# Kernel optimization log

Measured on AMD Instinct MI355X. Metric: run time of the kernel, lower is better.

The kernel has to match this reference:

```python
import jax, jax.numpy as jnp
import numpy as np

N_HEADS = 8


def _norm_weights(idx):
    # softmax over where(idx>0, 1, -9e15) along axis 1 -> uniform weights over non-pad slots
    logits = jnp.where(idx > 0, jnp.float32(1.0), jnp.float32(-9e15))
    return jax.nn.softmax(logits, axis=1)


def _layer_norm(x, g, b, eps=1e-6):
    mu = jnp.mean(x, axis=-1, keepdims=True)
    var = jnp.var(x, axis=-1, keepdims=True)
    return (x - mu) * jax.lax.rsqrt(var + eps) * g + b


def _mha_block(x, mask, wq, wk, wv, wo, g, b):
    # standard multi-head self-attention block with residual + layernorm
    B, L, D = x.shape
    hd = D // N_HEADS
    q = (x @ wq).reshape(B, L, N_HEADS, hd)
    k = (x @ wk).reshape(B, L, N_HEADS, hd)
    v = (x @ wv).reshape(B, L, N_HEADS, hd)
    scores = jnp.einsum('bqhd,bkhd->bhqk', q, k) / jnp.float32(np.sqrt(hd))
    scores = jnp.where(mask[:, None, None, :], jnp.float32(-1e9), scores)
    attn = jax.nn.softmax(scores, axis=-1)
    out = jnp.einsum('bhqk,bkhd->bqhd', attn, v).reshape(B, L, D) @ wo
    return _layer_norm(out + x, g, b)


def _forward(data_idx, seq, timestamps, user_level, useq, user_inf, user_cen,
             spread_status, id2vector,
             user_emb, cen_emb, time_emb, pos_emb, inf_emb,
             w1, w2, w3,
             t_wq, t_wk, t_wv, t_wo, t_g, t_b,
             s_wq, s_wk, s_wv, s_wo, s_g, s_b,
             W, W2, f_l1_w, f_l1_b, f_l2_w, f_l2_b, lin_w, lin_b):
    # ---- HGNN layer (hypergraph conv) ----
    tv = w3[0]  # TextVector = weight3[0]
    dot = w3 @ tv
    cos = dot / (jnp.linalg.norm(tv) * jnp.linalg.norm(w3, axis=1))
    inter_nw = jnp.mean(cos)  # scalar

    tweet_hidden = user_emb + cen_emb[user_cen]          # [N, D]
    x = (tweet_hidden @ w1) * inter_nw                   # [N, D]
    nor = _norm_weights(seq)                             # [E, L]
    edge = jnp.einsum('elc,el->ec', x[seq], nor)         # gather + weighted reduce
    edge = jax.nn.relu(edge)
    e1 = edge @ w2                                       # [E, D]
    u_nor = _norm_weights(useq)                          # [N, Lu]
    node = jnp.einsum('nlc,nl->nc', e1[useq], u_nor)     # [N, D]

    # ---- HGSL head ----
    sb = seq[data_idx]                                   # [B, L]
    nor_b = _norm_weights(sb)
    att_mask = sb == 0                                   # PAD == 0
    adj = node[sb]                                       # [B, L, D]

    att_hidden = adj + time_emb[timestamps[data_idx]]
    att_out = _mha_block(att_hidden, att_mask, t_wq, t_wk, t_wv, t_wo, t_g, t_b)
    news = jnp.einsum('blc,bl->bc', att_out, nor_b)
    news = jnp.concatenate([news, spread_status[data_idx][:, 2:] / 3600.0 / 24.0], axis=-1) @ W

    att_hidden_s = adj + inf_emb[user_inf[data_idx]] + pos_emb[user_level[data_idx]]
    att_out_s = _mha_block(att_hidden_s, att_mask, s_wq, s_wk, s_wv, s_wo, s_g, s_b)
    news_s = jnp.einsum('blc,bl->bc', att_out_s, nor_b)
    news_s = jnp.concatenate([news_s, spread_status[data_idx][:, :2]], axis=-1) @ W2

    # Gated fusion (linear3 unused in original forward; id2vector is overwritten/unused)
    emb = jnp.stack([news, news_s], axis=0)              # [2, B, D+2]
    score = jax.nn.softmax(jnp.tanh(emb @ f_l1_w + f_l1_b) @ f_l2_w + f_l2_b, axis=0)
    fused = jnp.sum(score * emb, axis=0)                 # [B, D+2]
    return jax.nn.log_softmax(fused @ lin_w + lin_b, axis=1)


def setup_inputs():
    key = jax.random.key(0)
    ks = jax.random.split(key, 40)
    N, E, L, Lu, D, B, TV = 50000, 10000, 50, 20, 128, 512, 768
    Dw = D + 2
    s = 0.05
    inp = {
        'data_idx': jax.random.randint(ks[0], (B,), 0, E),
        'seq': jax.random.randint(ks[1], (E, L), 0, N),
        'timestamps': jax.random.randint(ks[2], (E, L), 0, 5000),
        'user_level': jax.random.randint(ks[3], (E, L), 0, 50),
        'useq': jax.random.randint(ks[4], (N, Lu), 0, E),
        'user_inf': jax.random.randint(ks[5], (E, L), 0, 200),
        'user_cen': jax.random.randint(ks[6], (N,), 0, 600),
        'spread_status': jax.random.uniform(ks[7], (E, 4), dtype=jnp.float32),
        'id2vector': jax.random.normal(ks[8], (1,), dtype=jnp.float32),
        'user_emb': s * jax.random.normal(ks[9], (N, D), dtype=jnp.float32),
        'cen_emb': s * jax.random.normal(ks[10], (600, D), dtype=jnp.float32),
        'time_emb': s * jax.random.normal(ks[11], (5000, D), dtype=jnp.float32),
        'pos_emb': s * jax.random.normal(ks[12], (50, D), dtype=jnp.float32),
        'inf_emb': s * jax.random.normal(ks[13], (200, D), dtype=jnp.float32),
        'w1': s * jax.random.normal(ks[14], (D, D), dtype=jnp.float32),
        'w2': s * jax.random.normal(ks[15], (D, D), dtype=jnp.float32),
        'w3': s * jax.random.normal(ks[16], (TV, TV), dtype=jnp.float32),
        'W': s * jax.random.normal(ks[17], (Dw, Dw), dtype=jnp.float32),
        'W2': s * jax.random.normal(ks[18], (Dw, Dw), dtype=jnp.float32),
        'f_l1_w': s * jax.random.normal(ks[19], (Dw, Dw), dtype=jnp.float32),
        'f_l1_b': jnp.zeros((Dw,), jnp.float32),
        'f_l2_w': s * jax.random.normal(ks[20], (Dw, 1), dtype=jnp.float32),
        'f_l2_b': jnp.zeros((1,), jnp.float32),
        'lin_w': s * jax.random.normal(ks[21], (Dw, 2), dtype=jnp.float32),
        'lin_b': jnp.zeros((2,), jnp.float32),
    }
    for nm, i in [('t', 22), ('s', 27)]:
        inp[nm + '_wq'] = s * jax.random.normal(ks[i], (D, D), dtype=jnp.float32)
        inp[nm + '_wk'] = s * jax.random.normal(ks[i + 1], (D, D), dtype=jnp.float32)
        inp[nm + '_wv'] = s * jax.random.normal(ks[i + 2], (D, D), dtype=jnp.float32)
        inp[nm + '_wo'] = s * jax.random.normal(ks[i + 3], (D, D), dtype=jnp.float32)
        inp[nm + '_g'] = jnp.ones((D,), jnp.float32)
        inp[nm + '_b'] = jnp.zeros((D,), jnp.float32)
    return inp


def reference(data_idx, seq, timestamps, user_level, useq, user_inf, user_cen,
              spread_status, id2vector,
              user_emb, cen_emb, time_emb, pos_emb, inf_emb,
              w1, w2, w3,
              t_wq, t_wk, t_wv, t_wo, t_g, t_b,
              s_wq, s_wk, s_wv, s_wo, s_g, s_b,
              W, W2, f_l1_w, f_l1_b, f_l2_w, f_l2_b, lin_w, lin_b):
    return _forward(data_idx, seq, timestamps, user_level, useq, user_inf, user_cen,
                    spread_status, id2vector,
                    user_emb, cen_emb, time_emb, pos_emb, inf_emb,
                    w1, w2, w3,
                    t_wq, t_wk, t_wv, t_wo, t_g, t_b,
                    s_wq, s_wk, s_wv, s_wo, s_g, s_b,
                    W, W2, f_l1_w, f_l1_b, f_l2_w, f_l2_b, lin_w, lin_b)
```

## Files before the change

### kernel.cpp

```cpp
#include <hip/hip_runtime.h>
#include <math.h>

constexpr int Nn = 50000;
constexpr int Ee = 10000;
constexpr int Ll = 50;
constexpr int LuU = 20;
constexpr int Dd = 128;
constexpr int Bb = 512;
constexpr int TVv = 768;
constexpr int Dw = 130;
constexpr int BL = Bb * Ll;
constexpr int BLP = Bb * 64;

typedef __attribute__((ext_vector_type(8))) short bf8v;
typedef __attribute__((ext_vector_type(4))) float f4v;
typedef __attribute__((ext_vector_type(8))) unsigned short u16x8;
typedef __attribute__((ext_vector_type(4))) unsigned short u16x4;

__device__ __forceinline__ unsigned short f2bf(float f) {
  union { float f; unsigned u; } v; v.f = f;
  unsigned r = v.u + 0x7FFFu + ((v.u >> 16) & 1u);
  return (unsigned short)(r >> 16);
}
__device__ __forceinline__ float bf2f(unsigned short h) {
  union { unsigned u; float f; } v; v.u = ((unsigned)h) << 16; return v.f;
}
__device__ __forceinline__ int swz(int b) { return b ^ (((b >> 8) & 7) << 4); }
__device__ __forceinline__ int swz7(int b) { return b ^ (((b >> 7) & 7) << 4); }

__device__ __forceinline__ float block_sum_256(float v, volatile float* scr) {
#pragma unroll
  for (int o = 32; o > 0; o >>= 1) v += __shfl_down(v, o, 64);
  __syncthreads();
  if ((threadIdx.x & 63) == 0) scr[threadIdx.x >> 6] = v;
  __syncthreads();
  return scr[0] + scr[1] + scr[2] + scr[3];
}

__global__ __launch_bounds__(256) void k_cos(const float* __restrict__ w3,
                                             float* __restrict__ dotb,
                                             float* __restrict__ nrmb) {
  __shared__ float scr[4];
  int i = blockIdx.x;
  const float* row = w3 + (size_t)i * TVv;
  float d = 0.f, n = 0.f;
  for (int j = threadIdx.x; j < TVv; j += 256) {
    float a = row[j];
    d += a * w3[j];
    n += a * a;
  }
  d = block_sum_256(d, scr);
  n = block_sum_256(n, scr);
  if (threadIdx.x == 0) { dotb[i] = d; nrmb[i] = n; }
}

__global__ __launch_bounds__(256) void k_internw(const float* __restrict__ dotb,
                                                 const float* __restrict__ nrmb,
                                                 float* __restrict__ internw) {
  __shared__ float scr[4];
  float n0 = sqrtf(nrmb[0]);
  float s = 0.f;
  for (int i = threadIdx.x; i < TVv; i += 256)
    s += dotb[i] / (n0 * sqrtf(nrmb[i]));
  s = block_sum_256(s, scr);
  if (threadIdx.x == 0) *internw = s / (float)TVv;
}

__global__ __launch_bounds__(256) void k_prep(
    const float* w1, const float* w2,
    const float* twq, const float* twk, const float* twv, const float* two,
    const float* swq, const float* swk, const float* swv, const float* swo,
    unsigned short* __restrict__ out) {
  int wsel = blockIdx.x >> 3, part = blockIdx.x & 7;
  const float* w;
  switch (wsel) {
    case 0: w = w1; break;  case 1: w = w2; break;
    case 2: w = twq; break; case 3: w = twk; break;
    case 4: w = twv; break; case 5: w = two; break;
    case 6: w = swq; break; case 7: w = swk; break;
    case 8: w = swv; break; default: w = swo; break;
  }
  int u = part * 256 + threadIdx.x;
  int n = u >> 4, k0 = (u & 15) * 8;
  u16x8 pv;
#pragma unroll
  for (int i = 0; i < 8; i++) pv[i] = f2bf(w[(size_t)(k0 + i) * Dd + n]);
  ((u16x8*)(out + (size_t)wsel * Dd * Dd))[u] = pv;
}

template <int MODE>
__global__ __launch_bounds__(256) void k_gemm_plain(
    const void* __restrict__ inA, const float* __restrict__ in1,
    const int* __restrict__ gidx, const float* __restrict__ scalep,
    const unsigned short* __restrict__ WTg,
    unsigned short* __restrict__ out, int nrows) {
  __shared__ unsigned short WT[Dd * Dd];
  __shared__ __align__(16) unsigned short Ab[64 * Dd];
  int tid = threadIdx.x;
  {
    const u16x8* src = (const u16x8*)WTg;
    for (int u = tid; u < 2048; u += 256)
      *(u16x8*)((char*)WT + swz(u * 16)) = src[u];
  }
  int r0 = blockIdx.x * 64;
  if constexpr (MODE == 0) {
    float sc = *scalep;
    for (int u = tid; u < 1024; u += 256) {
      int rr = u >> 4, c0 = (u & 15) * 8;
      int r = r0 + rr;
      u16x8 pv;
      if (r < nrows) {
        const float* a = (const float*)inA + (size_t)r * Dd + c0;
        const float* c = in1 + (size_t)gidx[r] * Dd + c0;
#pragma unroll
        for (int i = 0; i < 8; i++) pv[i] = f2bf((a[i] + c[i]) * sc);
      } else {
#pragma unroll
        for (int i = 0; i < 8; i++) pv[i] = 0;
      }
      *(u16x8*)((char*)Ab + swz(rr * 256 + c0 * 2)) = pv;
    }
  } else {
    for (int u = tid; u < 1024; u += 256) {
      int rr = u >> 4;
      int r = r0 + rr;
      u16x8 pv;
      if (r < nrows) pv = ((const u16x8*)inA)[(size_t)r * 16 + (u & 15)];
      else {
#pragma unroll
        for (int i = 0; i < 8; i++) pv[i] = 0;
      }
      *(u16x8*)((char*)Ab + swz(rr * 256 + (u & 15) * 16)) = pv;
    }
  }
  __syncthreads();
  int lane = tid & 63, wid = tid >> 6;
  int lrow = lane & 15, lg = lane >> 4;
  bf8v af[4];
#pragma unroll
  for (int kc = 0; kc < 4; kc++)
    af[kc] = *(const bf8v*)((char*)Ab + swz((wid * 16 + lrow) * 256 + kc * 64 + lg * 16));
  f4v acc[8];
#pragma unroll
  for (int nt = 0; nt < 8; nt++)
#pragma unroll
    for (int j = 0; j < 4; j++) acc[nt][j] = 0.f;
#pragma unroll
  for (int nt = 0; nt < 8; nt++)
#pragma unroll
    for (int kc = 0; kc < 4; kc++) {
      bf8v bfg = *(const bf8v*)((char*)WT + swz((nt * 16 + lrow) * 256 + kc * 64 + lg * 16));
      acc[nt] = __builtin_amdgcn_mfma_f32_16x16x32_bf16(af[kc], bfg, acc[nt], 0, 0, 0);
    }
#pragma unroll
  for (int nt = 0; nt < 8; nt++)
#pragma unroll
    for (int j = 0; j < 4; j++) {
      int r = r0 + wid * 16 + lg * 4 + j;
      if (r < nrows) out[(size_t)r * Dd + nt * 16 + lrow] = f2bf(acc[nt][j]);
    }
}

__global__ __launch_bounds__(256) void k_gemm_qkv(
    const unsigned short* __restrict__ hidT, const unsigned short* __restrict__ hidS,
    const unsigned short* __restrict__ WTbase,
    unsigned short* __restrict__ Qp, unsigned short* __restrict__ Kp,
    unsigned short* __restrict__ VTp) {
  __shared__ unsigned short WT[Dd * Dd];
  __shared__ __align__(16) unsigned short Ab[128 * Dd];
  int tile = blockIdx.x & 255, branch = blockIdx.x >> 8;
  const unsigned short* in = branch ? hidS : hidT;
  int tid = threadIdx.x;
  for (int u = tid; u < 2048; u += 256) {
    int rr = u >> 4, ch = u & 15;
    int brow = rr >> 6, sub = rr & 63;
    u16x8 pv;
    if (sub < Ll)
      pv = ((const u16x8*)in)[(size_t)((tile * 2 + brow) * Ll + sub) * 16 + ch];
    else {
#pragma unroll
      for (int i = 0; i < 8; i++) pv[i] = 0;
    }
    *(u16x8*)((char*)Ab + swz(rr * 256 + ch * 16)) = pv;
  }
  {
    const u16x8* srcW = (const u16x8*)(WTbase + (size_t)(2 + branch * 4) * Dd * Dd);
    for (int u = tid; u < 2048; u += 256)
      *(u16x8*)((char*)WT + swz(u * 16)) = srcW[u];
  }
  __syncthreads();
  int lane = tid & 63, wid = tid >> 6;
  int lrow = lane & 15, lg = lane >> 4;
  bf8v af[2][4];
#pragma unroll
  for (int mi = 0; mi < 2; mi++)
#pragma unroll
    for (int kc = 0; kc < 4; kc++)
      af[mi][kc] = *(const bf8v*)((char*)Ab +
                    swz((wid * 32 + mi * 16 + lrow) * 256 + kc * 64 + lg * 16));
#pragma unroll 1
  for (int sel = 0; sel < 3; sel++) {
    f4v acc[2][8];
#pragma unroll
    for (int mi = 0; mi < 2; mi++)
#pragma unroll
      for (int nt = 0; nt < 8; nt++)
#pragma unroll
        for (int j = 0; j < 4; j++) acc[mi][nt][j] = 0.f;
#pragma unroll
    for (int nt = 0; nt < 8; nt++)
#pragma unroll
      for (int kc = 0; kc < 4; kc++) {
        bf8v bfg = *(const bf8v*)((char*)WT + swz((nt * 16 + lrow) * 256 + kc * 64 + lg * 16));
        acc[0][nt] = __builtin_amdgcn_mfma_f32_16x16x32_bf16(af[0][kc], bfg, acc[0][nt], 0, 0, 0);
        acc[1][nt] = __builtin_amdgcn_mfma_f32_16x16x32_bf16(af[1][kc], bfg, acc[1][nt], 0, 0, 0);
      }
    if (sel < 2) {
      unsigned short* outb = ((sel == 0) ? Qp : Kp) + (size_t)branch * BLP * Dd;
#pragma unroll
      for (int mi = 0; mi < 2; mi++)
#pragma unroll
        for (int nt = 0; nt < 8; nt++)
#pragma unroll
          for (int j = 0; j < 4; j++) {
            int r = tile * 128 + wid * 32 + mi * 16 + lg * 4 + j;
            outb[(size_t)r * Dd + nt * 16 + lrow] = f2bf(acc[mi][nt][j]);
          }
      __syncthreads();
      const u16x8* srcW = (const u16x8*)(WTbase + (size_t)(2 + branch * 4 + sel + 1) * Dd * Dd);
      for (int u = tid; u < 2048; u += 256)
        *(u16x8*)((char*)WT + swz(u * 16)) = srcW[u];
      __syncthreads();
    } else {
      __syncthreads();
#pragma unroll
      for (int mi = 0; mi < 2; mi++)
#pragma unroll
        for (int nt = 0; nt < 8; nt++) {
          int d = nt * 16 + lrow;
          int rl = wid * 32 + mi * 16 + lg * 4;
          u16x4 tv;
#pragma unroll
          for (int j = 0; j < 4; j++) tv[j] = f2bf(acc[mi][nt][j]);
          *(u16x4*)((char*)Ab + swz(d * 256 + rl * 2)) = tv;
        }
      __syncthreads();
      for (int u = tid; u < 2048; u += 256) {
        int d = u >> 4, ch = u & 15;
        u16x8 pv = *(const u16x8*)((char*)Ab + swz(d * 256 + ch * 16));
        int bidx = ch >> 3, kv0 = (ch & 7) * 8;
        *(u16x8*)(VTp + (((size_t)branch * Bb + tile * 2 + bidx) * Dd + d) * 64 + kv0) = pv;
      }
    }
  }
}

__global__ __launch_bounds__(256) void k_gemm_ln(
    const unsigned short* __restrict__ ctxp,
    const unsigned short* __restrict__ hidT, const unsigned short* __restrict__ hidS,
    const unsigned short* __restrict__ WTbase,
    const float* __restrict__ tg, const float* __restrict__ tb,
    const float* __restrict__ sg, const float* __restrict__ sb_,
    unsigned short* __restrict__ attall) {
  __shared__ unsigned short WT[Dd * Dd];
  __shared__ __align__(16) char UB[64 * 132 * 4];
  unsigned short* Ab = (unsigned short*)UB;
  float (*O)[132] = (float (*)[132])UB;

  int b = blockIdx.x & 511, branch = blockIdx.x >> 9;
  const unsigned short* resid = (branch ? hidS : hidT);
  const unsigned short* Wg = WTbase + (size_t)(5 + branch * 4) * Dd * Dd;
  const float* lng = branch ? sg : tg;
  const float* lnb = branch ? sb_ : tb;
  unsigned short* out = attall + (size_t)branch * BL * Dd;
  int tid = threadIdx.x;

  {
    const u16x8* src = (const u16x8*)Wg;
    for (int u = tid; u < 2048; u += 256)
      *(u16x8*)((char*)WT + swz(u * 16)) = src[u];
  }
  for (int u = tid; u < 1024; u += 256) {
    int rr = u >> 4;
    u16x8 pv = ((const u16x8*)ctxp)[(((size_t)branch * Bb + b) * 64 + rr) * 16 + (u & 15)];
    *(u16x8*)((char*)Ab + swz(rr * 256 + (u & 15) * 16)) = pv;
  }
  __syncthreads();

  int lane = tid & 63, wid = tid >> 6;
  int lrow = lane & 15, lg = lane >> 4;
  bf8v af[4];
#pragma unroll
  for (int kc = 0; kc < 4; kc++)
    af[kc] = *(const bf8v*)((char*)Ab + swz((wid * 16 + lrow) * 256 + kc * 64 + lg * 16));
  f4v acc[8];
#pragma unroll
  for (int nt = 0; nt < 8; nt++)
#pragma unroll
    for (int j = 0; j < 4; j++) acc[nt][j] = 0.f;
#pragma unroll
  for (int nt = 0; nt < 8; nt++)
#pragma unroll
    for (int kc = 0; kc < 4; kc++) {
      bf8v bfg = *(const bf8v*)((char*)WT + swz((nt * 16 + lrow) * 256 + kc * 64 + lg * 16));
      acc[nt] = __builtin_amdgcn_mfma_f32_16x16x32_bf16(af[kc], bfg, acc[nt], 0, 0, 0);
    }
  __syncthreads();
#pragma unroll
  for (int nt = 0; nt < 8; nt++)
#pragma unroll
    for (int j = 0; j < 4; j++)
      O[wid * 16 + lg * 4 + j][nt * 16 + lrow] = acc[nt][j];
  __syncthreads();
  int r = tid >> 2, c0 = (tid & 3) * 32;
  if (r < Ll) {
    size_t gr = (size_t)b * Ll + r;
    float vv[32];
    float s1 = 0.f, s2 = 0.f;
#pragma unroll
    for (int i8 = 0; i8 < 4; i8++) {
      u16x8 hb = *(const u16x8*)(resid + gr * Dd + c0 + i8 * 8);
#pragma unroll
      for (int i = 0; i < 8; i++) {
        float x = O[r][c0 + i8 * 8 + i] + bf2f(hb[i]);
        vv[i8 * 8 + i] = x; s1 += x; s2 += x * x;
      }
    }
    s1 += __shfl_xor(s1, 1, 64); s2 += __shfl_xor(s2, 1, 64);
    s1 += __shfl_xor(s1, 2, 64); s2 += __shfl_xor(s2, 2, 64);
    float mu = s1 * (1.f / Dd);
    float var = s2 * (1.f / Dd) - mu * mu;
    float rs = rsqrtf(var + 1e-6f);
#pragma unroll
    for (int i8 = 0; i8 < 4; i8++) {
      u16x8 ov;
#pragma unroll
      for (int i = 0; i < 8; i++) {
        int c = c0 + i8 * 8 + i;
        ov[i] = f2bf((vv[i8 * 8 + i] - mu) * rs * lng[c] + lnb[c]);
      }
      *(u16x8*)(out + gr * Dd + c0 + i8 * 8) = ov;
    }
  }
}

__global__ __launch_bounds__(256) void k_gather_e(const unsigned short* __restrict__ X,
                                                  const int* __restrict__ seq,
                                                  unsigned short* __restrict__ EDGE) {
  int r = blockIdx.x * 16 + (threadIdx.x >> 4);
  int c0 = (threadIdx.x & 15) * 8;
  const int* row = seq + (size_t)r * Ll;
  float acc[8];
#pragma unroll
  for (int i = 0; i < 8; i++) acc[i] = 0.f;
  int cnt = 0;
#pragma unroll 1
  for (int l0 = 0; l0 < Ll; l0 += 10) {
    int ids[10];
#pragma unroll
    for (int t = 0; t < 10; t++) ids[t] = row[l0 + t];
    u16x8 vv[10];
#pragma unroll
    for (int t = 0; t < 10; t++)
      vv[t] = *(const u16x8*)(X + (size_t)ids[t] * Dd + c0);
#pragma unroll
    for (int t = 0; t < 10; t++)
      if (ids[t] > 0) {
        cnt++;
#pragma unroll
        for (int i = 0; i < 8; i++) acc[i] += bf2f(vv[t][i]);
      }
  }
  u16x8 ov;
  if (cnt) {
    float inv = 1.f / (float)cnt;
#pragma unroll
    for (int i = 0; i < 8; i++) ov[i] = f2bf(fmaxf(acc[i] * inv, 0.f));
  } else {
    u16x8 x0 = *(const u16x8*)(X + c0);
#pragma unroll
    for (int i = 0; i < 8; i++) ov[i] = f2bf(fmaxf(bf2f(x0[i]), 0.f));
  }
  *(u16x8*)(EDGE + (size_t)r * Dd + c0) = ov;
}

__global__ __launch_bounds__(256) void k_hidfuse(
    const unsigned short* __restrict__ E1, const int* __restrict__ data_idx,
    const int* __restrict__ seq, const int* __restrict__ tsmp,
    const int* __restrict__ uinf, const int* __restrict__ ulev,
    const int* __restrict__ useq,
    const float* __restrict__ time_emb, const float* __restrict__ inf_emb,
    const float* __restrict__ pos_emb,
    unsigned short* __restrict__ hidTb, unsigned short* __restrict__ hidSb) {
  int bl = blockIdx.x * 16 + (threadIdx.x >> 4);
  int c0 = (threadIdx.x & 15) * 8;
  int b = bl / Ll, l = bl % Ll;
  int e = data_idx[b];
  int sid = seq[(size_t)e * Ll + l];
  const int* urow = useq + (size_t)sid * LuU;
  float acc[8];
#pragma unroll
  for (int i = 0; i < 8; i++) acc[i] = 0.f;
  int cnt = 0;
#pragma unroll 1
  for (int t0 = 0; t0 < LuU; t0 += 10) {
    int ids[10];
#pragma unroll
    for (int t = 0; t < 10; t++) ids[t] = urow[t0 + t];
    u16x8 vv[10];
#pragma unroll
    for (int t = 0; t < 10; t++)
      vv[t] = *(const u16x8*)(E1 + (size_t)ids[t] * Dd + c0);
#pragma unroll
    for (int t = 0; t < 10; t++)
      if (ids[t] > 0) {
        cnt++;
#pragma unroll
        for (int i = 0; i < 8; i++) acc[i] += bf2f(vv[t][i]);
      }
  }
  float node[8];
  if (cnt) {
    float inv = 1.f / (float)cnt;
#pragma unroll
    for (int i = 0; i < 8; i++) node[i] = acc[i] * inv;
  } else {
    u16x8 e0 = *(const u16x8*)(E1 + c0);
#pragma unroll
    for (int i = 0; i < 8; i++) node[i] = bf2f(e0[i]);
  }
  int ts = tsmp[(size_t)e * Ll + l];
  int fi = uinf[(size_t)e * Ll + l];
  int lv = ulev[(size_t)e * Ll + l];
  const float4* tp = (const float4*)(time_emb + (size_t)ts * Dd + c0);
  const float4* ip = (const float4*)(inf_emb + (size_t)fi * Dd + c0);
  const float4* pp = (const float4*)(pos_emb + (size_t)lv * Dd + c0);
  float4 t0 = tp[0], t1 = tp[1];
  float4 i0 = ip[0], i1 = ip[1];
  float4 p0 = pp[0], p1 = pp[1];
  float te[8] = {t0.x, t0.y, t0.z, t0.w, t1.x, t1.y, t1.z, t1.w};
  float ie[8] = {i0.x, i0.y, i0.z, i0.w, i1.x, i1.y, i1.z, i1.w};
  float pe[8] = {p0.x, p0.y, p0.z, p0.w, p1.x, p1.y, p1.z, p1.w};
  u16x8 ht, hs;
#pragma unroll
  for (int i = 0; i < 8; i++) {
    ht[i] = f2bf(node[i] + te[i]);
    hs[i] = f2bf(node[i] + ie[i] + pe[i]);
  }
  size_t o = (size_t)bl * Dd + c0;
  *(u16x8*)(hidTb + o) = ht;
  *(u16x8*)(hidSb + o) = hs;
}

__global__ __launch_bounds__(256, 4) void k_attn_mfma(
    const unsigned short* __restrict__ Qp,
    const unsigned short* __restrict__ Kp,
    const unsigned short* __restrict__ VTp,
    const int* __restrict__ data_idx,
    const int* __restrict__ seq,
    unsigned short* __restrict__ ctxp) {
  __shared__ __align__(16) char PTs[4 * 8192];
  __shared__ int maskl[Ll];
  int b = blockIdx.x, branch = blockIdx.y;
  int tid = threadIdx.x, lane = tid & 63, wid = tid >> 6;
  if (tid < Ll) maskl[tid] = (seq[(size_t)data_idx[b] * Ll + tid] == 0);
  __syncthreads();
  int lrow = lane & 15, lg = lane >> 4;
  size_t rbase = ((size_t)branch * Bb + b) * 64;
  size_t vrow  = ((size_t)branch * Bb + b) * Dd;
  char* PTw = PTs + wid * 8192;
#pragma unroll 1
  for (int hi = 0; hi < 2; hi++) {
    int h = wid * 2 + hi;
    bf8v af[4], bq[4];
    if (lg < 2) {
#pragma unroll
      for (int t = 0; t < 4; t++) {
        af[t] = *(const bf8v*)(Kp + (rbase + t * 16 + lrow) * Dd + h * 16 + lg * 8);
        bq[t] = *(const bf8v*)(Qp + (rbase + t * 16 + lrow) * Dd + h * 16 + lg * 8);
      }
    } else {
#pragma unroll
      for (int t = 0; t < 4; t++)
#pragma unroll
        for (int i = 0; i < 8; i++) { af[t][i] = 0; bq[t][i] = 0; }
    }
#pragma unroll 1
    for (int nt = 0; nt < 4; nt++) {
      f4v sa[4];
#pragma unroll
      for (int mt = 0; mt < 4; mt++)
#pragma unroll
        for (int j = 0; j < 4; j++) sa[mt][j] = 0.f;
#pragma unroll
      for (int mt = 0; mt < 4; mt++)
        sa[mt] = __builtin_amdgcn_mfma_f32_16x16x32_bf16(af[mt], bq[nt], sa[mt], 0, 0, 0);
      float m = -3.0e38f;
#pragma unroll
      for (int mt = 0; mt < 4; mt++)
#pragma unroll
        for (int j = 0; j < 4; j++) {
          int kk = mt * 16 + lg * 4 + j;
          int mk = (kk < Ll) ? maskl[kk] : 2;
          float v = sa[mt][j] * 0.25f;
          v = (mk == 1) ? -1e9f : v;
          v = (mk == 2) ? -3.0e38f : v;
          sa[mt][j] = v;
          m = fmaxf(m, v);
        }
      m = fmaxf(m, __shfl_xor(m, 16, 64));
      m = fmaxf(m, __shfl_xor(m, 32, 64));
      float s = 0.f;
#pragma unroll
      for (int mt = 0; mt < 4; mt++)
#pragma unroll
        for (int j = 0; j < 4; j++) {
          float p = expf(sa[mt][j] - m);
          sa[mt][j] = p;
          s += p;
        }
      s += __shfl_xor(s, 16, 64);
      s += __shfl_xor(s, 32, 64);
      float inv = 1.f / s;
      int q = nt * 16 + lrow;
#pragma unroll
      for (int mt = 0; mt < 4; mt++) {
        u16x4 pw;
#pragma unroll
        for (int j = 0; j < 4; j++) pw[j] = f2bf(sa[mt][j] * inv);
        *(u16x4*)(PTw + swz7(q * 128 + mt * 32 + lg * 8)) = pw;
      }
    }
    f4v pacc[4];
#pragma unroll
    for (int nt = 0; nt < 4; nt++)
#pragma unroll
      for (int j = 0; j < 4; j++) pacc[nt][j] = 0.f;
#pragma unroll
    for (int kt = 0; kt < 2; kt++) {
      bf8v av = *(const bf8v*)(VTp + (vrow + h * 16 + lrow) * 64 + kt * 32 + lg * 8);
#pragma unroll
      for (int nt = 0; nt < 4; nt++) {
        bf8v bv = *(const bf8v*)(PTw + swz7((nt * 16 + lrow) * 128 + kt * 64 + lg * 16));
        pacc[nt] = __builtin_amdgcn_mfma_f32_16x16x32_bf16(av, bv, pacc[nt], 0, 0, 0);
      }
    }
#pragma unroll
    for (int nt = 0; nt < 4; nt++) {
      int q = nt * 16 + lrow;
      unsigned* cp = (unsigned*)(ctxp + (rbase + q) * Dd + h * 16 + lg * 4);
      cp[0] = (unsigned)f2bf(pacc[nt][0]) | ((unsigned)f2bf(pacc[nt][1]) << 16);
      cp[1] = (unsigned)f2bf(pacc[nt][2]) | ((unsigned)f2bf(pacc[nt][3]) << 16);
    }
  }
}

__global__ __launch_bounds__(128) void k_newsred(const unsigned short* __restrict__ attall,
                                                 const int* __restrict__ data_idx,
                                                 const int* __restrict__ seq,
                                                 const float* __restrict__ spread,
                                                 float* __restrict__ news) {
  __shared__ int sl[Ll];
  __shared__ int scnt;
  int b = blockIdx.x, branch = blockIdx.y;
  int e = data_idx[b];
  const unsigned short* att = attall + (size_t)branch * BL * Dd;
  if (threadIdx.x < Ll) sl[threadIdx.x] = seq[(size_t)e * Ll + threadIdx.x];
  __syncthreads();
  if (threadIdx.x == 0) {
    int c = 0;
    for (int l = 0; l < Ll; l++) c += (sl[l] > 0);
    scnt = c;
  }
  __syncthreads();
  int cnt = scnt;
  float wnp = cnt ? 1.f / (float)cnt : 0.02f;
  int c = threadIdx.x;
  float acc = 0.f;
  for (int l = 0; l < Ll; l++) {
    float w = cnt ? ((sl[l] > 0) ? wnp : 0.f) : wnp;
    acc += w * bf2f(att[((size_t)b * Ll + l) * Dd + c]);
  }
  float* nrow = news + ((size_t)branch * Bb + b) * 132;
  nrow[c] = acc;
  if (c < 2) {
    nrow[Dd + c] = branch ? spread[(size_t)e * 4 + c]
                          : spread[(size_t)e * 4 + 2 + c] * (1.f / 86400.f);
  }
}

__global__ __launch_bounds__(256) void k_newsW(const float* __restrict__ news,
                                               const float* __restrict__ Wm,
                                               const float* __restrict__ W2m,
                                               float* __restrict__ NT,
                                               float* __restrict__ NS) {
  __shared__ float Wl[Dw][Dw + 1];
  __shared__ float nrow[132];
  int branch = blockIdx.y;
  const float* W = branch ? W2m : Wm;
  float* out = branch ? NS : NT;
  for (int u = threadIdx.x; u < Dw * Dw; u += 256)
    Wl[u / Dw][u % Dw] = W[u];
  for (int rr = 0; rr < 32; rr++) {
    int b = blockIdx.x * 32 + rr;
    __syncthreads();
    if (threadIdx.x < Dw)
      nrow[threadIdx.x] = news[((size_t)branch * Bb + b) * 132 + threadIdx.x];
    __syncthreads();
    int j = threadIdx.x;
    if (j < Dw) {
      float acc = 0.f;
      for (int kk = 0; kk < Dw; kk++) acc += nrow[kk] * Wl[kk][j];
      out[(size_t)b * Dw + j] = acc;
    }
  }
}

__global__ __launch_bounds__(256) void k_fusion(const float* __restrict__ nt,
                                                const float* __restrict__ ns,
                                                const float* __restrict__ l1w,
                                                const float* __restrict__ l1b,
                                                const float* __restrict__ l2w,
                                                const float* __restrict__ l2b,
                                                const float* __restrict__ linw,
                                                const float* __restrict__ linb,
                                                float* __restrict__ out) {
  __shared__ float rt[Dw], rs[Dw];
  __shared__ float scr[4];
  int b = blockIdx.x, j = threadIdx.x;
  if (j < Dw) { rt[j] = nt[(size_t)b * Dw + j]; rs[j] = ns[(size_t)b * Dw + j]; }
  __syncthreads();
  float pt = 0.f, ps = 0.f;
  if (j < Dw) {
    float at = l1b[j], as = l1b[j];
    for (int kk = 0; kk < Dw; kk++) {
      float w = l1w[(size_t)kk * Dw + j];
      at += rt[kk] * w;
      as += rs[kk] * w;
    }
    float lw2 = l2w[j];
    pt = tanhf(at) * lw2;
    ps = tanhf(as) * lw2;
  }
  float st = block_sum_256(pt, scr);
  float ss = block_sum_256(ps, scr);
  st += l2b[0]; ss += l2b[0];
  float m = fmaxf(st, ss);
  float e0 = expf(st - m), e1v = expf(ss - m);
  float inv = 1.f / (e0 + e1v);
  float s0 = e0 * inv, s1 = e1v * inv;
  float fj  = (j < Dw) ? (s0 * rt[j] + s1 * rs[j]) : 0.f;
  float w0  = (j < Dw) ? linw[(size_t)j * 2 + 0] : 0.f;
  float w1v = (j < Dw) ? linw[(size_t)j * 2 + 1] : 0.f;
  float l0 = block_sum_256(fj * w0, scr);
  float l1 = block_sum_256(fj * w1v, scr);
  if (j == 0) {
    l0 += linb[0]; l1 += linb[1];
    float mm = fmaxf(l0, l1);
    float lse = mm + logf(expf(l0 - mm) + expf(l1 - mm));
    out[(size_t)b * 2 + 0] = l0 - lse;
    out[(size_t)b * 2 + 1] = l1 - lse;
  }
}

extern "C" void kernel_launch(void* const* d_in, const int* in_sizes, int n_in,
                              void* d_out, int out_size, void* d_ws, size_t ws_size,
                              hipStream_t stream) {
  const int*   data_idx = (const int*)d_in[0];
  const int*   seq      = (const int*)d_in[1];
  const int*   tsmp     = (const int*)d_in[2];
  const int*   ulev     = (const int*)d_in[3];
  const int*   useq     = (const int*)d_in[4];
  const int*   uinf     = (const int*)d_in[5];
  const int*   ucen     = (const int*)d_in[6];
  const float* spread   = (const float*)d_in[7];
  const float* user_emb = (const float*)d_in[9];
  const float* cen_emb  = (const float*)d_in[10];
  const float* time_emb = (const float*)d_in[11];
  const float* pos_emb  = (const float*)d_in[12];
  const float* inf_emb  = (const float*)d_in[13];
  const float* w1       = (const float*)d_in[14];
  const float* w2       = (const float*)d_in[15];
  const float* w3       = (const float*)d_in[16];
  const float* Wm       = (const float*)d_in[17];
  const float* W2m      = (const float*)d_in[18];
  const float* f_l1_w   = (const float*)d_in[19];
  const float* f_l1_b   = (const float*)d_in[20];
  const float* f_l2_w   = (const float*)d_in[21];
  const float* f_l2_b   = (const float*)d_in[22];
  const float* lin_w    = (const float*)d_in[23];
  const float* lin_b    = (const float*)d_in[24];
  const float* t_wq = (const float*)d_in[25];
  const float* t_wk = (const float*)d_in[26];
  const float* t_wv = (const float*)d_in[27];
  const float* t_wo = (const float*)d_in[28];
  const float* t_g  = (const float*)d_in[29];
  const float* t_b  = (const float*)d_in[30];
  const float* s_wq = (const float*)d_in[31];
  const float* s_wk = (const float*)d_in[32];
  const float* s_wv = (const float*)d_in[33];
  const float* s_wo = (const float*)d_in[34];
  const float* s_g  = (const float*)d_in[35];
  const float* s_b  = (const float*)d_in[36];

  char* ws = (char*)d_ws;
  constexpr size_t SZ_WT  = (size_t)10 * Dd * Dd * 2;
  constexpr size_t SZ_XB  = (size_t)Nn * Dd * 2;
  constexpr size_t SZ_EB  = (size_t)Ee * Dd * 2;
  constexpr size_t SZ_BH  = (size_t)BL * Dd * 2;
  constexpr size_t SZ_PD  = (size_t)2 * BLP * Dd * 2;
  constexpr size_t OFF_WT  = 8192;
  constexpr size_t OFF_X   = OFF_WT + SZ_WT;
  constexpr size_t OFF_EDGE= OFF_X + SZ_XB;
  constexpr size_t OFF_E1  = OFF_EDGE + SZ_EB;
  constexpr size_t OFF_HTB = OFF_E1 + SZ_EB;
  constexpr size_t OFF_HSB = OFF_HTB + SZ_BH;
  constexpr size_t OFF_Q   = OFF_HSB + SZ_BH;
  constexpr size_t OFF_K   = OFF_Q + SZ_PD;
  constexpr size_t OFF_VT  = OFF_K + SZ_PD;
  constexpr size_t OFF_CTX = OFF_VT + SZ_PD;
  constexpr size_t OFF_ATT = OFF_Q;
  constexpr size_t OFF_NEWS= OFF_CTX + SZ_PD;
  constexpr size_t OFF_NT  = OFF_NEWS + (size_t)2 * Bb * 132 * 4;
  constexpr size_t OFF_NS  = OFF_NT + (size_t)Bb * Dw * 4;

  float* dotb    = (float*)(ws + 0);
  float* nrmb    = (float*)(ws + 3072);
  float* internw = (float*)(ws + 6144);
  unsigned short* WTall = (unsigned short*)(ws + OFF_WT);
  unsigned short* Xb    = (unsigned short*)(ws + OFF_X);
  unsigned short* EDGEb = (unsigned short*)(ws + OFF_EDGE);
  unsigned short* E1b   = (unsigned short*)(ws + OFF_E1);
  unsigned short* HIDTb = (unsigned short*)(ws + OFF_HTB);
  unsigned short* HIDSb = (unsigned short*)(ws + OFF_HSB);
  unsigned short* Qp    = (unsigned short*)(ws + OFF_Q);
  unsigned short* Kp    = (unsigned short*)(ws + OFF_K);
  unsigned short* VTp   = (unsigned short*)(ws + OFF_VT);
  unsigned short* CTXp  = (unsigned short*)(ws + OFF_CTX);
  unsigned short* ATTall= (unsigned short*)(ws + OFF_ATT);
  float*          NEWS  = (float*)(ws + OFF_NEWS);
  float*          NT    = (float*)(ws + OFF_NT);
  float*          NS    = (float*)(ws + OFF_NS);
  float* outp = (float*)d_out;

  k_prep<<<80, 256, 0, stream>>>(w1, w2, t_wq, t_wk, t_wv, t_wo,
                                 s_wq, s_wk, s_wv, s_wo, WTall);
  k_cos<<<TVv, 256, 0, stream>>>(w3, dotb, nrmb);
  k_internw<<<1, 256, 0, stream>>>(dotb, nrmb, internw);

  k_gemm_plain<0><<<(Nn + 63) / 64, 256, 0, stream>>>(
      user_emb, cen_emb, ucen, internw, WTall + 0 * Dd * Dd, Xb, Nn);
  k_gather_e<<<Ee / 16, 256, 0, stream>>>(Xb, seq, EDGEb);
  k_gemm_plain<1><<<(Ee + 63) / 64, 256, 0, stream>>>(
      EDGEb, nullptr, nullptr, nullptr, WTall + 1 * Dd * Dd, E1b, Ee);
  k_hidfuse<<<BL / 16, 256, 0, stream>>>(E1b, data_idx, seq, tsmp, uinf, ulev, useq,
                                         time_emb, inf_emb, pos_emb, HIDTb, HIDSb);

  k_gemm_qkv<<<512, 256, 0, stream>>>(HIDTb, HIDSb, WTall, Qp, Kp, VTp);
  k_attn_mfma<<<dim3(Bb, 2), 256, 0, stream>>>(Qp, Kp, VTp, data_idx, seq, CTXp);
  k_gemm_ln<<<1024, 256, 0, stream>>>(CTXp, HIDTb, HIDSb, WTall,
                                      t_g, t_b, s_g, s_b, ATTall);

  k_newsred<<<dim3(Bb, 2), 128, 0, stream>>>(ATTall, data_idx, seq, spread, NEWS);
  k_newsW<<<dim3(16, 2), 256, 0, stream>>>(NEWS, Wm, W2m, NT, NS);
  k_fusion<<<Bb, 256, 0, stream>>>(NT, NS, f_l1_w, f_l1_b, f_l2_w, f_l2_b,
                                   lin_w, lin_b, outp);

  (void)in_sizes; (void)n_in; (void)out_size; (void)ws_size;
}
```

Baseline: 378.1 us.

## Fuse QKV projection and attention into one per-sequence kernel

Merges the QKV GEMM kernel and the attention kernel into a single kernel with one block per (batch, branch). Q, K and V^T stay in LDS instead of round-tripping through global memory, and the mask is built through lane shuffles rather than an LDS table. In exchange, each block now reloads all three 128x128 weight matrices for only 64 rows, and the 80KB of LDS caps occupancy at about two blocks per CU.

```diff
diff --git a/kernel.cpp b/kernel.cpp
--- a/kernel.cpp
+++ b/kernel.cpp
@@ -161,96 +161,216 @@
     }
 }
 
-__global__ __launch_bounds__(256) void k_gemm_qkv(
+__global__ __launch_bounds__(256, 2) void k_qkvattn(
     const unsigned short* __restrict__ hidT, const unsigned short* __restrict__ hidS,
     const unsigned short* __restrict__ WTbase,
-    unsigned short* __restrict__ Qp, unsigned short* __restrict__ Kp,
-    unsigned short* __restrict__ VTp) {
-  __shared__ unsigned short WT[Dd * Dd];
-  __shared__ __align__(16) unsigned short Ab[128 * Dd];
-  int tile = blockIdx.x & 255, branch = blockIdx.x >> 8;
-  const unsigned short* in = branch ? hidS : hidT;
-  int tid = threadIdx.x;
-  for (int u = tid; u < 2048; u += 256) {
+    const int* __restrict__ data_idx, const int* __restrict__ seq,
+    unsigned short* __restrict__ ctxp) {
+  __shared__ __align__(16) char LDS[81920];
+  unsigned short* AQ  = (unsigned short*)(LDS);
+  unsigned short* WP  = (unsigned short*)(LDS + 16384);
+  unsigned short* Ks  = (unsigned short*)(LDS + 49152);
+  unsigned short* VTs = (unsigned short*)(LDS + 65536);
+
+  int b = blockIdx.x, branch = blockIdx.y;
+  int tid = threadIdx.x, lane = tid & 63, wid = tid >> 6;
+  int lrow = lane & 15, lg = lane >> 4;
+  const unsigned short* hid = (branch ? hidS : hidT) + (size_t)b * Ll * Dd;
+
+  int e = data_idx[b];
+  int mi = (lane < Ll) ? (seq[(size_t)e * Ll + lane] == 0 ? 1 : 0) : 2;
+  int mflag[4][4];
+#pragma unroll
+  for (int mt = 0; mt < 4; mt++)
+#pragma unroll
+    for (int j = 0; j < 4; j++)
+      mflag[mt][j] = __shfl(mi, mt * 16 + lg * 4 + j, 64);
+
+  for (int u = tid; u < 1024; u += 256) {
     int rr = u >> 4, ch = u & 15;
-    int brow = rr >> 6, sub = rr & 63;
     u16x8 pv;
-    if (sub < Ll)
-      pv = ((const u16x8*)in)[(size_t)((tile * 2 + brow) * Ll + sub) * 16 + ch];
+    if (rr < Ll) pv = *(const u16x8*)(hid + (size_t)rr * Dd + ch * 8);
     else {
 #pragma unroll
       for (int i = 0; i < 8; i++) pv[i] = 0;
     }
-    *(u16x8*)((char*)Ab + swz(rr * 256 + ch * 16)) = pv;
+    *(u16x8*)((char*)AQ + swz(rr * 256 + ch * 16)) = pv;
   }
   {
     const u16x8* srcW = (const u16x8*)(WTbase + (size_t)(2 + branch * 4) * Dd * Dd);
     for (int u = tid; u < 2048; u += 256)
-      *(u16x8*)((char*)WT + swz(u * 16)) = srcW[u];
-  }
-  __syncthreads();
-  int lane = tid & 63, wid = tid >> 6;
-  int lrow = lane & 15, lg = lane >> 4;
-  bf8v af[2][4];
-#pragma unroll
-  for (int mi = 0; mi < 2; mi++)
-#pragma unroll
-    for (int kc = 0; kc < 4; kc++)
-      af[mi][kc] = *(const bf8v*)((char*)Ab +
-                    swz((wid * 32 + mi * 16 + lrow) * 256 + kc * 64 + lg * 16));
+      *(u16x8*)((char*)WP + swz(u * 16)) = srcW[u];
+  }
+  __syncthreads();
+  bf8v hf[4];
+#pragma unroll
+  for (int kc = 0; kc < 4; kc++)
+    hf[kc] = *(const bf8v*)((char*)AQ + swz((wid * 16 + lrow) * 256 + kc * 64 + lg * 16));
+  __syncthreads();
+
+  {
+    f4v acc[8];
+#pragma unroll
+    for (int nt = 0; nt < 8; nt++)
+#pragma unroll
+      for (int j = 0; j < 4; j++) acc[nt][j] = 0.f;
+#pragma unroll
+    for (int nt = 0; nt < 8; nt++)
+#pragma unroll
+      for (int kc = 0; kc < 4; kc++) {
+        bf8v wf = *(const bf8v*)((char*)WP + swz((nt * 16 + lrow) * 256 + kc * 64 + lg * 16));
+        acc[nt] = __builtin_amdgcn_mfma_f32_16x16x32_bf16(wf, hf[kc], acc[nt], 0, 0, 0);
+      }
+    __syncthreads();
+#pragma unroll
+    for (int nt = 0; nt < 8; nt++) {
+      u16x4 qv;
+#pragma unroll
+      for (int j = 0; j < 4; j++) qv[j] = f2bf(acc[nt][j]);
+      *(u16x4*)((char*)AQ + swz((wid * 16 + lrow) * 256 + (nt * 16 + lg * 4) * 2)) = qv;
+    }
+  }
+  {
+    const u16x8* srcW = (const u16x8*)(WTbase + (size_t)(3 + branch * 4) * Dd * Dd);
+    for (int u = tid; u < 2048; u += 256)
+      *(u16x8*)((char*)WP + swz(u * 16)) = srcW[u];
+  }
+  __syncthreads();
+  {
+    f4v acc[8];
+#pragma unroll
+    for (int nt = 0; nt < 8; nt++)
+#pragma unroll
+      for (int j = 0; j < 4; j++) acc[nt][j] = 0.f;
+#pragma unroll
+    for (int nt = 0; nt < 8; nt++)
+#pragma unroll
+      for (int kc = 0; kc < 4; kc++) {
+        bf8v wf = *(const bf8v*)((char*)WP + swz((nt * 16 + lrow) * 256 + kc * 64 + lg * 16));
+        acc[nt] = __builtin_amdgcn_mfma_f32_16x16x32_bf16(wf, hf[kc], acc[nt], 0, 0, 0);
+      }
+    __syncthreads();
+#pragma unroll
+    for (int nt = 0; nt < 8; nt++) {
+      u16x4 kv4;
+#pragma unroll
+      for (int j = 0; j < 4; j++) kv4[j] = f2bf(acc[nt][j]);
+      *(u16x4*)((char*)Ks + swz((wid * 16 + lrow) * 256 + (nt * 16 + lg * 4) * 2)) = kv4;
+    }
+  }
+  {
+    const u16x8* srcW = (const u16x8*)(WTbase + (size_t)(4 + branch * 4) * Dd * Dd);
+    for (int u = tid; u < 2048; u += 256)
+      *(u16x8*)((char*)WP + swz(u * 16)) = srcW[u];
+  }
+  __syncthreads();
+  {
+    f4v acc[8];
+#pragma unroll
+    for (int nt = 0; nt < 8; nt++)
+#pragma unroll
+      for (int j = 0; j < 4; j++) acc[nt][j] = 0.f;
+#pragma unroll
+    for (int nt = 0; nt < 8; nt++)
+#pragma unroll
+      for (int kc = 0; kc < 4; kc++) {
+        bf8v wf = *(const bf8v*)((char*)WP + swz((nt * 16 + lrow) * 256 + kc * 64 + lg * 16));
+        acc[nt] = __builtin_amdgcn_mfma_f32_16x16x32_bf16(hf[kc], wf, acc[nt], 0, 0, 0);
+      }
+    __syncthreads();
+#pragma unroll
+    for (int nt = 0; nt < 8; nt++) {
+      u16x4 tv;
+#pragma unroll
+      for (int j = 0; j < 4; j++) tv[j] = f2bf(acc[nt][j]);
+      *(u16x4*)((char*)VTs + swz7((nt * 16 + lrow) * 128 + (wid * 16 + lg * 4) * 2)) = tv;
+    }
+  }
+  __syncthreads();
+
+  char* PTw = (char*)WP + wid * 8192;
+  size_t rbase = ((size_t)branch * Bb + b) * 64;
 #pragma unroll 1
-  for (int sel = 0; sel < 3; sel++) {
-    f4v acc[2][8];
-#pragma unroll
-    for (int mi = 0; mi < 2; mi++)
-#pragma unroll
-      for (int nt = 0; nt < 8; nt++)
-#pragma unroll
-        for (int j = 0; j < 4; j++) acc[mi][nt][j] = 0.f;
-#pragma unroll
-    for (int nt = 0; nt < 8; nt++)
-#pragma unroll
-      for (int kc = 0; kc < 4; kc++) {
-        bf8v bfg = *(const bf8v*)((char*)WT + swz((nt * 16 + lrow) * 256 + kc * 64 + lg * 16));
-        acc[0][nt] = __builtin_amdgcn_mfma_f32_16x16x32_bf16(af[0][kc], bfg, acc[0][nt], 0, 0, 0);
-        acc[1][nt] = __builtin_amdgcn_mfma_f32_16x16x32_bf16(af[1][kc], bfg, acc[1][nt], 0, 0, 0);
-      }
-    if (sel < 2) {
-      unsigned short* outb = ((sel == 0) ? Qp : Kp) + (size_t)branch * BLP * Dd;
-#pragma unroll
-      for (int mi = 0; mi < 2; mi++)
-#pragma unroll
-        for (int nt = 0; nt < 8; nt++)
-#pragma unroll
-          for (int j = 0; j < 4; j++) {
-            int r = tile * 128 + wid * 32 + mi * 16 + lg * 4 + j;
-            outb[(size_t)r * Dd + nt * 16 + lrow] = f2bf(acc[mi][nt][j]);
-          }
-      __syncthreads();
-      const u16x8* srcW = (const u16x8*)(WTbase + (size_t)(2 + branch * 4 + sel + 1) * Dd * Dd);
-      for (int u = tid; u < 2048; u += 256)
-        *(u16x8*)((char*)WT + swz(u * 16)) = srcW[u];
-      __syncthreads();
+  for (int hi = 0; hi < 2; hi++) {
+    int h = wid * 2 + hi;
+    bf8v af[4], bq[4];
+    if (lg < 2) {
+#pragma unroll
+      for (int t = 0; t < 4; t++) {
+        af[t] = *(const bf8v*)((char*)Ks + swz((t * 16 + lrow) * 256 + h * 32 + lg * 16));
+        bq[t] = *(const bf8v*)((char*)AQ + swz((t * 16 + lrow) * 256 + h * 32 + lg * 16));
+      }
     } else {
-      __syncthreads();
-#pragma unroll
-      for (int mi = 0; mi < 2; mi++)
-#pragma unroll
-        for (int nt = 0; nt < 8; nt++) {
-          int d = nt * 16 + lrow;
-          int rl = wid * 32 + mi * 16 + lg * 4;
-          u16x4 tv;
-#pragma unroll
-          for (int j = 0; j < 4; j++) tv[j] = f2bf(acc[mi][nt][j]);
-          *(u16x4*)((char*)Ab + swz(d * 256 + rl * 2)) = tv;
+#pragma unroll
+      for (int t = 0; t < 4; t++)
+#pragma unroll
+        for (int i = 0; i < 8; i++) { af[t][i] = 0; bq[t][i] = 0; }
+    }
+#pragma unroll 1
+    for (int nt = 0; nt < 4; nt++) {
+      f4v sa[4];
+#pragma unroll
+      for (int mt = 0; mt < 4; mt++)
+#pragma unroll
+        for (int j = 0; j < 4; j++) sa[mt][j] = 0.f;
+#pragma unroll
+      for (int mt = 0; mt < 4; mt++)
+        sa[mt] = __builtin_amdgcn_mfma_f32_16x16x32_bf16(af[mt], bq[nt], sa[mt], 0, 0, 0);
+      float m = -3.0e38f;
+#pragma unroll
+      for (int mt = 0; mt < 4; mt++)
+#pragma unroll
+        for (int j = 0; j < 4; j++) {
+          int mk = mflag[mt][j];
+          float v = sa[mt][j] * 0.25f;
+          v = (mk == 1) ? -1e9f : v;
+          v = (mk == 2) ? -3.0e38f : v;
+          sa[mt][j] = v;
+          m = fmaxf(m, v);
         }
-      __syncthreads();
-      for (int u = tid; u < 2048; u += 256) {
-        int d = u >> 4, ch = u & 15;
-        u16x8 pv = *(const u16x8*)((char*)Ab + swz(d * 256 + ch * 16));
-        int bidx = ch >> 3, kv0 = (ch & 7) * 8;
-        *(u16x8*)(VTp + (((size_t)branch * Bb + tile * 2 + bidx) * Dd + d) * 64 + kv0) = pv;
-      }
+      m = fmaxf(m, __shfl_xor(m, 16, 64));
+      m = fmaxf(m, __shfl_xor(m, 32, 64));
+      float s = 0.f;
+#pragma unroll
+      for (int mt = 0; mt < 4; mt++)
+#pragma unroll
+        for (int j = 0; j < 4; j++) {
+          float p = expf(sa[mt][j] - m);
+          sa[mt][j] = p;
+          s += p;
+        }
+      s += __shfl_xor(s, 16, 64);
+      s += __shfl_xor(s, 32, 64);
+      float inv = 1.f / s;
+      int q = nt * 16 + lrow;
+#pragma unroll
+      for (int mt = 0; mt < 4; mt++) {
+        u16x4 pw;
+#pragma unroll
+        for (int j = 0; j < 4; j++) pw[j] = f2bf(sa[mt][j] * inv);
+        *(u16x4*)(PTw + swz7(q * 128 + mt * 32 + lg * 8)) = pw;
+      }
+    }
+    f4v pacc[4];
+#pragma unroll
+    for (int nt = 0; nt < 4; nt++)
+#pragma unroll
+      for (int j = 0; j < 4; j++) pacc[nt][j] = 0.f;
+#pragma unroll
+    for (int kt = 0; kt < 2; kt++) {
+      bf8v av = *(const bf8v*)((char*)VTs + swz7((h * 16 + lrow) * 128 + kt * 64 + lg * 16));
+#pragma unroll
+      for (int nt = 0; nt < 4; nt++) {
+        bf8v bv = *(const bf8v*)(PTw + swz7((nt * 16 + lrow) * 128 + kt * 64 + lg * 16));
+        pacc[nt] = __builtin_amdgcn_mfma_f32_16x16x32_bf16(av, bv, pacc[nt], 0, 0, 0);
+      }
+    }
+#pragma unroll
+    for (int nt = 0; nt < 4; nt++) {
+      int q = nt * 16 + lrow;
+      unsigned* cp = (unsigned*)(ctxp + (rbase + q) * Dd + h * 16 + lg * 4);
+      cp[0] = (unsigned)f2bf(pacc[nt][0]) | ((unsigned)f2bf(pacc[nt][1]) << 16);
+      cp[1] = (unsigned)f2bf(pacc[nt][2]) | ((unsigned)f2bf(pacc[nt][3]) << 16);
     }
   }
 }
@@ -450,109 +570,6 @@
   size_t o = (size_t)bl * Dd + c0;
   *(u16x8*)(hidTb + o) = ht;
   *(u16x8*)(hidSb + o) = hs;
-}
-
-__global__ __launch_bounds__(256, 4) void k_attn_mfma(
-    const unsigned short* __restrict__ Qp,
-    const unsigned short* __restrict__ Kp,
-    const unsigned short* __restrict__ VTp,
-    const int* __restrict__ data_idx,
-    const int* __restrict__ seq,
-    unsigned short* __restrict__ ctxp) {
-  __shared__ __align__(16) char PTs[4 * 8192];
-  __shared__ int maskl[Ll];
-  int b = blockIdx.x, branch = blockIdx.y;
-  int tid = threadIdx.x, lane = tid & 63, wid = tid >> 6;
-  if (tid < Ll) maskl[tid] = (seq[(size_t)data_idx[b] * Ll + tid] == 0);
-  __syncthreads();
-  int lrow = lane & 15, lg = lane >> 4;
-  size_t rbase = ((size_t)branch * Bb + b) * 64;
-  size_t vrow  = ((size_t)branch * Bb + b) * Dd;
-  char* PTw = PTs + wid * 8192;
-#pragma unroll 1
-  for (int hi = 0; hi < 2; hi++) {
-    int h = wid * 2 + hi;
-    bf8v af[4], bq[4];
-    if (lg < 2) {
-#pragma unroll
-      for (int t = 0; t < 4; t++) {
-        af[t] = *(const bf8v*)(Kp + (rbase + t * 16 + lrow) * Dd + h * 16 + lg * 8);
-        bq[t] = *(const bf8v*)(Qp + (rbase + t * 16 + lrow) * Dd + h * 16 + lg * 8);
-      }
-    } else {
-#pragma unroll
-      for (int t = 0; t < 4; t++)
-#pragma unroll
-        for (int i = 0; i < 8; i++) { af[t][i] = 0; bq[t][i] = 0; }
-    }
-#pragma unroll 1
-    for (int nt = 0; nt < 4; nt++) {
-      f4v sa[4];
-#pragma unroll
-      for (int mt = 0; mt < 4; mt++)
-#pragma unroll
-        for (int j = 0; j < 4; j++) sa[mt][j] = 0.f;
-#pragma unroll
-      for (int mt = 0; mt < 4; mt++)
-        sa[mt] = __builtin_amdgcn_mfma_f32_16x16x32_bf16(af[mt], bq[nt], sa[mt], 0, 0, 0);
-      float m = -3.0e38f;
-#pragma unroll
-      for (int mt = 0; mt < 4; mt++)
-#pragma unroll
-        for (int j = 0; j < 4; j++) {
-          int kk = mt * 16 + lg * 4 + j;
-          int mk = (kk < Ll) ? maskl[kk] : 2;
-          float v = sa[mt][j] * 0.25f;
-          v = (mk == 1) ? -1e9f : v;
-          v = (mk == 2) ? -3.0e38f : v;
-          sa[mt][j] = v;
-          m = fmaxf(m, v);
-        }
-      m = fmaxf(m, __shfl_xor(m, 16, 64));
-      m = fmaxf(m, __shfl_xor(m, 32, 64));
-      float s = 0.f;
-#pragma unroll
-      for (int mt = 0; mt < 4; mt++)
-#pragma unroll
-        for (int j = 0; j < 4; j++) {
-          float p = expf(sa[mt][j] - m);
-          sa[mt][j] = p;
-          s += p;
-        }
-      s += __shfl_xor(s, 16, 64);
-      s += __shfl_xor(s, 32, 64);
-      float inv = 1.f / s;
-      int q = nt * 16 + lrow;
-#pragma unroll
-      for (int mt = 0; mt < 4; mt++) {
-        u16x4 pw;
-#pragma unroll
-        for (int j = 0; j < 4; j++) pw[j] = f2bf(sa[mt][j] * inv);
-        *(u16x4*)(PTw + swz7(q * 128 + mt * 32 + lg * 8)) = pw;
-      }
-    }
-    f4v pacc[4];
-#pragma unroll
-    for (int nt = 0; nt < 4; nt++)
-#pragma unroll
-      for (int j = 0; j < 4; j++) pacc[nt][j] = 0.f;
-#pragma unroll
-    for (int kt = 0; kt < 2; kt++) {
-      bf8v av = *(const bf8v*)(VTp + (vrow + h * 16 + lrow) * 64 + kt * 32 + lg * 8);
-#pragma unroll
-      for (int nt = 0; nt < 4; nt++) {
-        bf8v bv = *(const bf8v*)(PTw + swz7((nt * 16 + lrow) * 128 + kt * 64 + lg * 16));
-        pacc[nt] = __builtin_amdgcn_mfma_f32_16x16x32_bf16(av, bv, pacc[nt], 0, 0, 0);
-      }
-    }
-#pragma unroll
-    for (int nt = 0; nt < 4; nt++) {
-      int q = nt * 16 + lrow;
-      unsigned* cp = (unsigned*)(ctxp + (rbase + q) * Dd + h * 16 + lg * 4);
-      cp[0] = (unsigned)f2bf(pacc[nt][0]) | ((unsigned)f2bf(pacc[nt][1]) << 16);
-      cp[1] = (unsigned)f2bf(pacc[nt][2]) | ((unsigned)f2bf(pacc[nt][3]) << 16);
-    }
-  }
 }
 
 __global__ __launch_bounds__(128) void k_newsred(const unsigned short* __restrict__ attall,
@@ -715,12 +732,9 @@
   constexpr size_t OFF_E1  = OFF_EDGE + SZ_EB;
   constexpr size_t OFF_HTB = OFF_E1 + SZ_EB;
   constexpr size_t OFF_HSB = OFF_HTB + SZ_BH;
-  constexpr size_t OFF_Q   = OFF_HSB + SZ_BH;
-  constexpr size_t OFF_K   = OFF_Q + SZ_PD;
-  constexpr size_t OFF_VT  = OFF_K + SZ_PD;
-  constexpr size_t OFF_CTX = OFF_VT + SZ_PD;
-  constexpr size_t OFF_ATT = OFF_Q;
-  constexpr size_t OFF_NEWS= OFF_CTX + SZ_PD;
+  constexpr size_t OFF_CTX = OFF_HSB + SZ_BH;
+  constexpr size_t OFF_ATT = OFF_CTX + SZ_PD;
+  constexpr size_t OFF_NEWS= OFF_ATT + 2 * SZ_BH;
   constexpr size_t OFF_NT  = OFF_NEWS + (size_t)2 * Bb * 132 * 4;
   constexpr size_t OFF_NS  = OFF_NT + (size_t)Bb * Dw * 4;
 
@@ -733,9 +747,6 @@
   unsigned short* E1b   = (unsigned short*)(ws + OFF_E1);
   unsigned short* HIDTb = (unsigned short*)(ws + OFF_HTB);
   unsigned short* HIDSb = (unsigned short*)(ws + OFF_HSB);
-  unsigned short* Qp    = (unsigned short*)(ws + OFF_Q);
-  unsigned short* Kp    = (unsigned short*)(ws + OFF_K);
-  unsigned short* VTp   = (unsigned short*)(ws + OFF_VT);
   unsigned short* CTXp  = (unsigned short*)(ws + OFF_CTX);
   unsigned short* ATTall= (unsigned short*)(ws + OFF_ATT);
   float*          NEWS  = (float*)(ws + OFF_NEWS);
@@ -756,8 +767,7 @@
   k_hidfuse<<<BL / 16, 256, 0, stream>>>(E1b, data_idx, seq, tsmp, uinf, ulev, useq,
                                          time_emb, inf_emb, pos_emb, HIDTb, HIDSb);
 
-  k_gemm_qkv<<<512, 256, 0, stream>>>(HIDTb, HIDSb, WTall, Qp, Kp, VTp);
-  k_attn_mfma<<<dim3(Bb, 2), 256, 0, stream>>>(Qp, Kp, VTp, data_idx, seq, CTXp);
+  k_qkvattn<<<dim3(Bb, 2), 256, 0, stream>>>(HIDTb, HIDSb, WTall, data_idx, seq, CTXp);
   k_gemm_ln<<<1024, 256, 0, stream>>>(CTXp, HIDTb, HIDSb, WTall,
                                       t_g, t_b, s_g, s_b, ATTall);
 
```

Result: faster. 366.0 us (-3.2%).
